# Optimization experiments

Hardware: AMD Instinct MI355X
Metric: run time of the kernel (lower is better)

The kernel has to match this reference:

```python
import jax, jax.numpy as jnp
import numpy as np

NUM_HEADS = 16

def setup_inputs() -> dict:
    key = jax.random.key(0)
    k1, k2, k3 = jax.random.split(key, 3)
    B, N, C = 2, 2048, 1024
    x = jax.random.normal(k1, (B, N, C), dtype=jnp.float32)
    # Dense layers: qkv (C -> 3C, no bias), proj (C -> C, with bias)
    w_qkv = jax.random.normal(k2, (C, 3 * C), dtype=jnp.float32) * (C ** -0.5)
    w_proj = jax.random.normal(k3, (C, C), dtype=jnp.float32) * (C ** -0.5)
    b_proj = jnp.zeros((C,), dtype=jnp.float32)
    return {"x": x, "w_qkv": w_qkv, "w_proj": w_proj, "b_proj": b_proj}

def reference(x, w_qkv, w_proj, b_proj):
    B, N, C = x.shape
    H = NUM_HEADS
    Dh = C // H
    scale = Dh ** -0.5
    qkv = x @ w_qkv                                   # [B,N,3C]
    qkv = qkv.reshape(B, N, 3, H, Dh)
    qkv = jnp.transpose(qkv, (2, 0, 3, 1, 4))         # [3,B,H,N,Dh]
    q, k, v = qkv[0], qkv[1], qkv[2]
    attn = jnp.einsum('bhnd,bhmd->bhnm', q, k) * scale  # [B,H,N,N]
    attn = jax.nn.softmax(attn, axis=-1)
    out = jnp.einsum('bhnm,bhmd->bhnd', attn, v)        # [B,H,N,Dh]
    out = jnp.transpose(out, (0, 2, 1, 3)).reshape(B, N, C)
    return out @ w_proj + b_proj
```

## Files before the change

### kernel.cpp

```cpp
#include <hip/hip_runtime.h>
#include <stdint.h>


typedef unsigned short u16;
typedef uint32_t u32;
typedef __bf16 bf16x8 __attribute__((ext_vector_type(8)));
typedef unsigned short u16x8 __attribute__((ext_vector_type(8)));
typedef float f32x4 __attribute__((ext_vector_type(4)));
typedef float f32x16 __attribute__((ext_vector_type(16)));
typedef uint32_t u32x4v __attribute__((ext_vector_type(4)));

#define DEV static __device__ __forceinline__

DEV u16 f2bf(float f) {
    uint32_t u = __float_as_uint(f);
    u += 0x7fffu + ((u >> 16) & 1u);
    return (u16)(u >> 16);
}

DEV u32 cvtpk(float lo, float hi_) {
    u32 r;
    asm("v_cvt_pk_bf16_f32 %0, %1, %2" : "=v"(r) : "v"(lo), "v"(hi_));
    return r;
}
DEV void plswap(u32& x, u32& y) {
    asm("v_permlane32_swap_b32 %0, %1" : "+v"(x), "+v"(y));
}
DEV float exp2f_fast(float x) {
    float r;
    asm("v_exp_f32 %0, %1" : "=v"(r) : "v"(x));
    return r;
}

DEV void gload_lds16(const void* g, void* l) {
    __builtin_amdgcn_global_load_lds(
        (const __attribute__((address_space(1))) uint32_t*)g,
        (__attribute__((address_space(3))) uint32_t*)l, 16, 0, 0);
}

#define WAIT_VM(N) asm volatile("s_waitcnt vmcnt(" #N ")" ::: "memory")
#define RAW_BAR() __builtin_amdgcn_s_barrier()
#define SCHED_PIN() __builtin_amdgcn_sched_barrier(0)

DEV bf16x8 swz_load16(const u16* base, int row, int kbyte) {
    int off = (row * 128 + kbyte) ^ ((row & 7) << 4);
    return *reinterpret_cast<const bf16x8*>(reinterpret_cast<const char*>(base) + off);
}

__global__ __launch_bounds__(256) void prep_kernel(
    const float* __restrict__ x, u16* __restrict__ xb,
    const float* __restrict__ wq, u16* __restrict__ wqt,
    const float* __restrict__ wp, u16* __restrict__ wpt) {
    __shared__ float T[32][33];
    int b = blockIdx.x, tid = threadIdx.x;
    if (b < 2048) {
        int t = b * 256 + tid;
        const float4* p = reinterpret_cast<const float4*>(x) + (size_t)t * 2;
        float4 a = p[0], c = p[1];
        u16x8 o;
        o[0] = f2bf(a.x); o[1] = f2bf(a.y); o[2] = f2bf(a.z); o[3] = f2bf(a.w);
        o[4] = f2bf(c.x); o[5] = f2bf(c.y); o[6] = f2bf(c.z); o[7] = f2bf(c.w);
        reinterpret_cast<u16x8*>(xb)[t] = o;
        return;
    }
    const float* in;
    u16* out;
    int bx, by, R = 1024, Cc;
    if (b < 5120) {
        int idx = b - 2048;
        bx = idx % 96; by = idx / 96; Cc = 3072; in = wq; out = wqt;
    } else {
        int idx = b - 5120;
        bx = idx % 32; by = idx / 32; Cc = 1024; in = wp; out = wpt;
    }
    int tx = tid & 31, ty = tid >> 5;
    int xcol = bx * 32 + tx;
    int y0 = by * 32;
#pragma unroll
    for (int i = 0; i < 4; i++) {
        int y = y0 + ty + i * 8;
        T[ty + i * 8][tx] = in[(size_t)y * Cc + xcol];
    }
    __syncthreads();
    int xo = y0 + tx;
    int yo0 = bx * 32;
#pragma unroll
    for (int i = 0; i < 4; i++) {
        int yo = yo0 + ty + i * 8;
        out[(size_t)yo * R + xo] = f2bf(T[tx][ty + i * 8]);
    }
}

__global__ void trv_kernel(const u16* __restrict__ v, u16* __restrict__ vt) {
    __shared__ u16 T[64][72];
    int bh = blockIdx.y, t = blockIdx.x, tid = threadIdx.x;
    const u16* vb = v + (size_t)bh * 2048 * 64;
    u16* vo = vt + (size_t)bh * 64 * 2048;
#pragma unroll
    for (int i = 0; i < 2; i++) {
        int c = tid + i * 256, row = c >> 3, c8 = c & 7;
        u16x8 a = *reinterpret_cast<const u16x8*>(vb + (size_t)(t * 64 + row) * 64 + c8 * 8);
#pragma unroll
        for (int j = 0; j < 8; j++) T[row][c8 * 8 + j] = a[j];
    }
    __syncthreads();
#pragma unroll
    for (int i = 0; i < 2; i++) {
        int c = tid + i * 256, drow = c >> 3, c8 = c & 7;
        u16x8 o;
#pragma unroll
        for (int j = 0; j < 8; j++) o[j] = T[c8 * 8 + j][drow];
        *reinterpret_cast<u16x8*>(vo + (size_t)drow * 2048 + t * 64 + c8 * 8) = o;
    }
}


template <int EPI>
__global__ __launch_bounds__(256, 2) void gemm_kernel(
    const u16* __restrict__ A, const u16* __restrict__ Bt, int ntiles,
    u16* __restrict__ o_q, u16* __restrict__ o_k, u16* __restrict__ o_v,
    float* __restrict__ o_f, const float* __restrict__ bias) {
    __shared__ __align__(16) u16 Al[2][8192];
    __shared__ __align__(16) u16 Bl[2][8192];
    int tid = threadIdx.x;
    int bm = blockIdx.x / ntiles, bn = blockIdx.x % ntiles;
    int lane = tid & 63, w = tid >> 6;
    int wr = w >> 1, wc = w & 1;
    int l15 = lane & 15, lhi = lane >> 4;

    f32x4 acc[4][4];
#pragma unroll
    for (int i = 0; i < 4; i++)
#pragma unroll
        for (int j = 0; j < 4; j++) acc[i][j] = (f32x4){0.f, 0.f, 0.f, 0.f};

#define GSTAGE(bb, kt_)                                                                       \
    {                                                                                         \
        _Pragma("unroll") for (int i = 0; i < 4; i++) {                                       \
            int lin = w * 4096 + i * 1024 + lane * 16;                                        \
            int row = lin >> 7;                                                               \
            int src = (lin & 127) ^ ((row & 7) << 4);                                         \
            gload_lds16((const char*)A + (size_t)(bm * 128 + row) * 2048 + (size_t)(kt_)*128 + src, \
                        (char*)Al[bb] + lin);                                                 \
            gload_lds16((const char*)Bt + (size_t)(bn * 128 + row) * 2048 + (size_t)(kt_)*128 + src, \
                        (char*)Bl[bb] + lin);                                                 \
        }                                                                                     \
    }

    GSTAGE(0, 0);

    for (int kt = 0; kt < 16; ++kt) {
        int cur = kt & 1;
        if (kt < 15) {
            GSTAGE(cur ^ 1, kt + 1);
            WAIT_VM(8);
        } else {
            WAIT_VM(0);
        }
        RAW_BAR();
        SCHED_PIN();
#pragma unroll
        for (int ks = 0; ks < 2; ++ks) {
            bf16x8 af[4], bfr[4];
#pragma unroll
            for (int mi = 0; mi < 4; ++mi) af[mi] = swz_load16(Al[cur], wr * 64 + mi * 16 + l15, ks * 64 + lhi * 16);
#pragma unroll
            for (int ni = 0; ni < 4; ++ni) bfr[ni] = swz_load16(Bl[cur], wc * 64 + ni * 16 + l15, ks * 64 + lhi * 16);
            __builtin_amdgcn_s_setprio(1);
#pragma unroll
            for (int mi = 0; mi < 4; ++mi)
#pragma unroll
                for (int ni = 0; ni < 4; ++ni)
                    acc[mi][ni] = __builtin_amdgcn_mfma_f32_16x16x32_bf16(af[mi], bfr[ni], acc[mi][ni], 0, 0, 0);
            __builtin_amdgcn_s_setprio(0);
        }
        RAW_BAR();
    }
#undef GSTAGE

    int row0 = bm * 128 + wr * 64, col0 = bn * 128 + wc * 64;
    if (EPI == 0) {
#pragma unroll
        for (int mi = 0; mi < 4; mi++)
#pragma unroll
            for (int ni = 0; ni < 4; ni++) {
                int col = col0 + ni * 16 + l15;
                int sel = col >> 10, cc = col & 1023;
                int h = cc >> 6, d = cc & 63;
#pragma unroll
                for (int j = 0; j < 4; j++) {
                    int r = row0 + mi * 16 + lhi * 4 + j;
                    int b = r >> 11, n = r & 2047;
                    size_t idx = (((size_t)(b * 16 + h)) * 2048 + n) * 64 + d;
                    float v = acc[mi][ni][j];
                    if (sel == 0) o_q[idx] = f2bf(v * 0.18033688f);
                    else if (sel == 1) o_k[idx] = f2bf(v);
                    else o_v[idx] = f2bf(v);
                }
            }
    } else {
#pragma unroll
        for (int mi = 0; mi < 4; mi++)
#pragma unroll
            for (int ni = 0; ni < 4; ni++) {
                int col = col0 + ni * 16 + l15;
                float bb = bias[col];
#pragma unroll
                for (int j = 0; j < 4; j++) {
                    int r = row0 + mi * 16 + lhi * 4 + j;
                    o_f[(size_t)r * 1024 + col] = acc[mi][ni][j] + bb;
                }
            }
    }
}

__global__ __launch_bounds__(512, 4) void flash6_kernel(
    const u16* __restrict__ qg, const u16* __restrict__ kg, const u16* __restrict__ vtg,
    u16* __restrict__ o) {
    __shared__ __align__(16) char smem[65536];

    int tid = threadIdx.x, lane = tid & 63, w = tid >> 6;
    int wg = w & 3, g = w >> 2;
    int l31 = lane & 31, hi = lane >> 5;
    int p = blockIdx.y * 16 + blockIdx.x;
    int bh = p & 31, qt = p >> 5;
    int q0 = qt * 128 + wg * 32;

#define KL(gg, bb) (smem + ((gg) * 2 + (bb)) * 8192)
#define VL(gg, bb) (smem + 32768 + ((gg) * 2 + (bb)) * 8192)

    const u16* qp = qg + ((size_t)bh * 2048 + q0 + l31) * 64 + hi * 8;
    bf16x8 qf[4];
#pragma unroll
    for (int ds = 0; ds < 4; ds++) qf[ds] = *reinterpret_cast<const bf16x8*>(qp + ds * 16);

    const char* kbg = (const char*)(kg + (size_t)bh * 2048 * 64) + (size_t)g * 16 * 8192;
    const char* vbg = (const char*)(vtg + (size_t)bh * 64 * 2048) + (size_t)g * 2048;

    int srow = lane >> 1, sinner = (lane & 1) * 16;
    int fbase = l31 * 32 + hi * 16;

#define STAGE(bb, tt)                                                                     \
    {                                                                                     \
        _Pragma("unroll") for (int i = 0; i < 2; i++) {                                   \
            gload_lds16(kbg + (size_t)(tt) * 8192 + (i * 32 + srow) * 128 + wg * 32 + sinner, \
                        KL(g, bb) + wg * 2048 + i * 1024 + lane * 16);                    \
            gload_lds16(vbg + (size_t)(i * 32 + srow) * 4096 + (size_t)(tt) * 128 + wg * 32 + sinner, \
                        VL(g, bb) + wg * 2048 + i * 1024 + lane * 16);                    \
        }                                                                                 \
    }

    f32x16 accO[2];
#pragma unroll
    for (int db = 0; db < 2; db++)
#pragma unroll
        for (int r = 0; r < 16; r++) accO[db][r] = 0.f;
    float lsum = 0.f;

    STAGE(0, 0);

    for (int pp = 0; pp < 16; ++pp) {
        int c = pp & 1;
        if (pp < 15) {
            STAGE(c ^ 1, pp + 1);
            WAIT_VM(4);
        } else {
            WAIT_VM(0);
        }
        RAW_BAR();
        SCHED_PIN();

        bf16x8 ka[2][4];
#pragma unroll
        for (int kvb = 0; kvb < 2; kvb++)
#pragma unroll
            for (int ds = 0; ds < 4; ds++)
                ka[kvb][ds] = *reinterpret_cast<const bf16x8*>(KL(g, c) + ds * 2048 + kvb * 1024 + fbase);
        f32x16 s[2];
        __builtin_amdgcn_s_setprio(1);
#pragma unroll
        for (int kvb = 0; kvb < 2; kvb++) {
#pragma unroll
            for (int r = 0; r < 16; r++) s[kvb][r] = 0.f;
#pragma unroll
            for (int ds = 0; ds < 4; ds++)
                s[kvb] = __builtin_amdgcn_mfma_f32_32x32x16_bf16(ka[kvb][ds], qf[ds], s[kvb], 0, 0, 0);
        }
        __builtin_amdgcn_s_setprio(0);

#pragma unroll
        for (int kvb = 0; kvb < 2; kvb++)
#pragma unroll
            for (int r = 0; r < 16; r++) s[kvb][r] = exp2f_fast(s[kvb][r]);
        float t_[8];
#pragma unroll
        for (int r = 0; r < 8; r++)
            t_[r] = (s[0][r] + s[0][r + 8]) + (s[1][r] + s[1][r + 8]);
#pragma unroll
        for (int r = 0; r < 4; r++) t_[r] += t_[r + 4];
        lsum += (t_[0] + t_[1]) + (t_[2] + t_[3]);

        bf16x8 pb[4];
#pragma unroll
        for (int kvb = 0; kvb < 2; kvb++) {
            u32 x0 = cvtpk(s[kvb][0], s[kvb][1]), y0 = cvtpk(s[kvb][4], s[kvb][5]);
            u32 x1 = cvtpk(s[kvb][2], s[kvb][3]), y1 = cvtpk(s[kvb][6], s[kvb][7]);
            u32 x2 = cvtpk(s[kvb][8], s[kvb][9]), y2 = cvtpk(s[kvb][12], s[kvb][13]);
            u32 x3 = cvtpk(s[kvb][10], s[kvb][11]), y3 = cvtpk(s[kvb][14], s[kvb][15]);
            plswap(x0, y0); plswap(x1, y1); plswap(x2, y2); plswap(x3, y3);
            u32x4v plo = {x0, x1, y0, y1};
            u32x4v phi = {x2, x3, y2, y3};
            pb[2 * kvb] = __builtin_bit_cast(bf16x8, plo);
            pb[2 * kvb + 1] = __builtin_bit_cast(bf16x8, phi);
        }

        bf16x8 va[2][4];
#pragma unroll
        for (int db = 0; db < 2; db++)
#pragma unroll
            for (int ks = 0; ks < 4; ks++)
                va[db][ks] = *reinterpret_cast<const bf16x8*>(VL(g, c) + ks * 2048 + db * 1024 + fbase);
        __builtin_amdgcn_s_setprio(1);
#pragma unroll
        for (int db = 0; db < 2; db++)
#pragma unroll
            for (int ks = 0; ks < 4; ks++)
                accO[db] = __builtin_amdgcn_mfma_f32_32x32x16_bf16(va[db][ks], pb[ks], accO[db], 0, 0, 0);
        __builtin_amdgcn_s_setprio(0);

        RAW_BAR();
    }
#undef STAGE

    lsum += __shfl_xor(lsum, 32);

    float* mbuf = (float*)smem;
    int base = (wg * 64 + lane) * 36;
    if (g == 1) {
#pragma unroll
        for (int db = 0; db < 2; db++)
#pragma unroll
            for (int q4 = 0; q4 < 4; q4++) {
                f32x4 v4 = {accO[db][q4 * 4 + 0], accO[db][q4 * 4 + 1],
                            accO[db][q4 * 4 + 2], accO[db][q4 * 4 + 3]};
                *reinterpret_cast<f32x4*>(mbuf + base + db * 16 + q4 * 4) = v4;
            }
        mbuf[base + 32] = lsum;
    }
    __syncthreads();
    if (g == 0) {
        float lsum2 = mbuf[base + 32];
        float inv = 1.f / (lsum + lsum2);
        int b = bh >> 4, h = bh & 15;
        u16* ob = o + ((size_t)(b * 2048 + q0 + l31)) * 1024 + h * 64;
#pragma unroll
        for (int db = 0; db < 2; db++) {
            f32x4 m4[4];
#pragma unroll
            for (int q4 = 0; q4 < 4; q4++)
                m4[q4] = *reinterpret_cast<const f32x4*>(mbuf + base + db * 16 + q4 * 4);
#pragma unroll
            for (int i = 0; i < 8; i++) {
                int r = 2 * i;
                int d = (r & 3) + 8 * (r >> 2) + 4 * hi + 32 * db;
                float lo = (accO[db][r] + m4[r >> 2][r & 3]) * inv;
                float hi_ = (accO[db][r + 1] + m4[(r + 1) >> 2][(r + 1) & 3]) * inv;
                *reinterpret_cast<u32*>(ob + d) = cvtpk(lo, hi_);
            }
        }
    }
#undef KL
#undef VL
}


extern "C" void kernel_launch(void* const* d_in, const int* in_sizes, int n_in,
                              void* d_out, int out_size, void* d_ws, size_t ws_size,
                              hipStream_t stream) {
    (void)in_sizes; (void)n_in; (void)out_size; (void)ws_size;
    const float* x = (const float*)d_in[0];
    const float* w_qkv = (const float*)d_in[1];
    const float* w_proj = (const float*)d_in[2];
    const float* b_proj = (const float*)d_in[3];
    float* out = (float*)d_out;
    char* ws = (char*)d_ws;

    u16* xb   = (u16*)(ws + 0);
    u16* wqt  = (u16*)(ws + 8388608);
    u16* wpt  = (u16*)(ws + 14680064);
    u16* qws  = (u16*)(ws + 16777216);
    u16* kws  = (u16*)(ws + 25165824);
    u16* vws  = (u16*)(ws + 33554432);
    u16* vtws = (u16*)(ws + 41943040);
    u16* attn = (u16*)(ws + 50331648);

    prep_kernel<<<6144, 256, 0, stream>>>(x, xb, w_qkv, wqt, w_proj, wpt);
    gemm_kernel<0><<<32 * 24, 256, 0, stream>>>(xb, wqt, 24, qws, kws, vws, nullptr, nullptr);
    trv_kernel<<<dim3(32, 32), 256, 0, stream>>>(vws, vtws);
    flash6_kernel<<<dim3(16, 32), 512, 0, stream>>>(qws, kws, vtws, attn);
    gemm_kernel<1><<<32 * 8, 256, 0, stream>>>(attn, wpt, 8, nullptr, nullptr, nullptr, out, b_proj);
}
```

Before: 117.7 us.

## Drop GEMM LDS double buffering and remap blocks per XCD

```diff
diff --git a/kernel.cpp b/kernel.cpp
--- a/kernel.cpp
+++ b/kernel.cpp
@@ -120,10 +120,12 @@
     const u16* __restrict__ A, const u16* __restrict__ Bt, int ntiles,
     u16* __restrict__ o_q, u16* __restrict__ o_k, u16* __restrict__ o_v,
     float* __restrict__ o_f, const float* __restrict__ bias) {
-    __shared__ __align__(16) u16 Al[2][8192];
-    __shared__ __align__(16) u16 Bl[2][8192];
+    __shared__ __align__(16) u16 Al[8192];
+    __shared__ __align__(16) u16 Bl[8192];
     int tid = threadIdx.x;
-    int bm = blockIdx.x / ntiles, bn = blockIdx.x % ntiles;
+    int p = blockIdx.x;
+    int xcd = p & 7, q = p >> 3;
+    int bm = xcd * 4 + q / ntiles, bn = q % ntiles;
     int lane = tid & 63, w = tid >> 6;
     int wr = w >> 1, wc = w & 1;
     int l15 = lane & 15, lhi = lane >> 4;
@@ -134,38 +136,25 @@
 #pragma unroll
         for (int j = 0; j < 4; j++) acc[i][j] = (f32x4){0.f, 0.f, 0.f, 0.f};
 
-#define GSTAGE(bb, kt_)                                                                       \
-    {                                                                                         \
-        _Pragma("unroll") for (int i = 0; i < 4; i++) {                                       \
-            int lin = w * 4096 + i * 1024 + lane * 16;                                        \
-            int row = lin >> 7;                                                               \
-            int src = (lin & 127) ^ ((row & 7) << 4);                                         \
-            gload_lds16((const char*)A + (size_t)(bm * 128 + row) * 2048 + (size_t)(kt_)*128 + src, \
-                        (char*)Al[bb] + lin);                                                 \
-            gload_lds16((const char*)Bt + (size_t)(bn * 128 + row) * 2048 + (size_t)(kt_)*128 + src, \
-                        (char*)Bl[bb] + lin);                                                 \
-        }                                                                                     \
-    }
-
-    GSTAGE(0, 0);
-
     for (int kt = 0; kt < 16; ++kt) {
-        int cur = kt & 1;
-        if (kt < 15) {
-            GSTAGE(cur ^ 1, kt + 1);
-            WAIT_VM(8);
-        } else {
-            WAIT_VM(0);
-        }
-        RAW_BAR();
-        SCHED_PIN();
+#pragma unroll
+        for (int i = 0; i < 4; i++) {
+            int lin = w * 4096 + i * 1024 + lane * 16;
+            int row = lin >> 7;
+            int src = (lin & 127) ^ ((row & 7) << 4);
+            gload_lds16((const char*)A + (size_t)(bm * 128 + row) * 2048 + (size_t)kt * 128 + src,
+                        (char*)Al + lin);
+            gload_lds16((const char*)Bt + (size_t)(bn * 128 + row) * 2048 + (size_t)kt * 128 + src,
+                        (char*)Bl + lin);
+        }
+        __syncthreads();
 #pragma unroll
         for (int ks = 0; ks < 2; ++ks) {
             bf16x8 af[4], bfr[4];
 #pragma unroll
-            for (int mi = 0; mi < 4; ++mi) af[mi] = swz_load16(Al[cur], wr * 64 + mi * 16 + l15, ks * 64 + lhi * 16);
-#pragma unroll
-            for (int ni = 0; ni < 4; ++ni) bfr[ni] = swz_load16(Bl[cur], wc * 64 + ni * 16 + l15, ks * 64 + lhi * 16);
+            for (int mi = 0; mi < 4; ++mi) af[mi] = swz_load16(Al, wr * 64 + mi * 16 + l15, ks * 64 + lhi * 16);
+#pragma unroll
+            for (int ni = 0; ni < 4; ++ni) bfr[ni] = swz_load16(Bl, wc * 64 + ni * 16 + l15, ks * 64 + lhi * 16);
             __builtin_amdgcn_s_setprio(1);
 #pragma unroll
             for (int mi = 0; mi < 4; ++mi)
@@ -174,9 +163,8 @@
                     acc[mi][ni] = __builtin_amdgcn_mfma_f32_16x16x32_bf16(af[mi], bfr[ni], acc[mi][ni], 0, 0, 0);
             __builtin_amdgcn_s_setprio(0);
         }
-        RAW_BAR();
-    }
-#undef GSTAGE
+        __syncthreads();
+    }
 
     int row0 = bm * 128 + wr * 64, col0 = bn * 128 + wc * 64;
     if (EPI == 0) {
```

After: 107.7 us. 8.5% less time.
